# Performance work log

Hardware: AMD Instinct MI355X
Metric: run time of the kernel (lower is better)

The kernel has to match this reference:

```python
import jax, jax.numpy as jnp
import numpy as np

EPS = 1e-5
TOP_N = 8
NUM_POINTS = 100
OUT_LO, OUT_HI = 0.0, 1.0


def setup_inputs() -> dict:
    key = jax.random.key(0)
    ks = jax.random.split(key, 7)
    B, D, M, R, MO = 2048, 8, 7, 32768, 9
    x = jax.random.normal(ks[0], (B, D), dtype=jnp.float32)
    # antecedent MF index per (rule, input); -1 means input unused in that rule
    antecedents = jax.random.randint(ks[1], (R, D), 0, M + 1) - 1  # values in [-1, M)
    consequents = jax.random.randint(ks[2], (R,), 0, MO)
    in_centers = jax.random.normal(ks[3], (D, M), dtype=jnp.float32)
    in_widths = 0.2 + 0.3 * jax.random.uniform(ks[4], (D, M), dtype=jnp.float32)
    out_centers = jax.random.uniform(ks[5], (MO,), dtype=jnp.float32)
    out_widths = 0.05 + 0.2 * jax.random.uniform(ks[6], (MO,), dtype=jnp.float32)
    return {"x": x, "antecedents": antecedents, "consequents": consequents,
            "in_centers": in_centers, "in_widths": in_widths,
            "out_centers": out_centers, "out_widths": out_widths}


def reference(x, antecedents, consequents, in_centers, in_widths, out_centers, out_widths):
    B, D = x.shape
    R = antecedents.shape[0]
    M = in_centers.shape[1]

    # Fuzzification: Gaussian input MFs, clamped like the torch module. mu: [B, D, M]
    z = (x[:, :, None] - in_centers[None, :, :]) / in_widths[None, :, :]
    mu = jnp.clip(jnp.exp(-0.5 * z * z), EPS, 1.0)

    # Rule firing strengths: product over inputs of selected memberships ([B, R]).
    # Small fixed loop over D (8) keeps peak memory at one [B, R] temp per step.
    firing = jnp.ones((B, R), dtype=x.dtype)
    for i in range(D):
        idx = antecedents[:, i]                      # [R], -1 => unused
        safe = jnp.clip(idx, 0, M - 1)
        vals = mu[:, i, safe]                        # [B, R]
        firing = firing * jnp.where(idx[None, :] == -1, jnp.ones((), x.dtype), vals)

    top_vals, top_idx = jax.lax.top_k(firing, TOP_N)  # [B, TOP_N]

    # Output universe and output MF table: [MO, P]
    universe = jnp.linspace(OUT_LO, OUT_HI, NUM_POINTS, dtype=x.dtype)
    zo = (universe[None, :] - out_centers[:, None]) / out_widths[:, None]
    out_mu = jnp.exp(-0.5 * zo * zo)

    # Mamdani implication (product) + aggregation (sum) + centroid defuzzification
    cons_top = consequents[top_idx]                   # [B, TOP_N]
    implications = top_vals[:, :, None] * out_mu[cons_top]  # [B, TOP_N, P]
    aggregated = implications.sum(axis=1)             # [B, P]
    numerator = (universe[None, :] * aggregated).sum(axis=1)
    denominator = aggregated.sum(axis=1) + EPS
    return numerator / denominator
```

## Files before the change

kernel.cpp:

```cpp
#include <hip/hip_runtime.h>
#include <math.h>

#define DD 8
#define MM 7
#define MOO 9
#define NPTS 100
#define EPSF 1e-5f

#define THREADS 1024
#define ITERS 8
#define ROWS 8
#define CAP 256
#define THR_SLACK 0.9879f

__device__ __forceinline__ float bl(unsigned u) { return __uint_as_float(u << 16); }
__device__ __forceinline__ float bh(unsigned u) { return __uint_as_float(u & 0xFFFF0000u); }
__device__ __forceinline__ unsigned pkb(float a, float b) {
    return (__float_as_uint(b) & 0xFFFF0000u) | (__float_as_uint(a) >> 16);
}

__global__ __launch_bounds__(256) void pack_kernel(const int* __restrict__ ant,
                                                   unsigned* __restrict__ g_off,
                                                   int R) {
    int r = blockIdx.x * 256 + threadIdx.x;
    if (r < R) {
        const int4* a = reinterpret_cast<const int4*>(ant) + (size_t)r * 2;
        int4 lo = a[0], hi = a[1];
        int v[8] = {lo.x, lo.y, lo.z, lo.w, hi.x, hi.y, hi.z, hi.w};
        unsigned code = 0u;
        #pragma unroll
        for (int i = 0; i < 8; ++i) {
            int c = v[i];
            c = (c < 0) ? 7 : (c > MM - 1 ? MM - 1 : c);
            code |= (unsigned)c << (3 * i);
        }
        g_off[r] = ((code & 4095u) << 3) | ((((code >> 12) << 3) + 32768u) << 16);
    }
}

__global__ __launch_bounds__(THREADS, 4) void anfis_fused8(
    const float* __restrict__ x,
    const unsigned* __restrict__ stream_off,
    const int* __restrict__ consequents,
    const float* __restrict__ in_centers,
    const float* __restrict__ in_widths,
    const float* __restrict__ out_centers,
    const float* __restrict__ out_widths,
    float* __restrict__ out)
{
    __shared__ uint4 quads[8192];
    __shared__ float mu[ROWS][64];
    __shared__ float pairs[ROWS][256];
    __shared__ uint4 smaxpk[THREADS];
    __shared__ float s0s[MOO], s1s[MOO];
    __shared__ float sT[ROWS];
    __shared__ int   scnt[ROWS];
    __shared__ int   wlcnt;
    __shared__ float wv[ROWS][8];
    __shared__ int   wc[ROWS][8];

    const int tid = threadIdx.x;
    const int b0  = blockIdx.x * ROWS;

    unsigned short* wl = (unsigned short*)quads;
    float* cvals = (float*)(quads + 1024);
    int*   cidx  = (int*)(quads + 1536);

    if (tid < 512) {
        int row = tid >> 6, d = (tid >> 3) & 7, c = tid & 7;
        float v = 1.0f;
        if (c < MM) {
            float z = (x[(b0 + row) * DD + d] - in_centers[d * MM + c]) / in_widths[d * MM + c];
            v = expf(-0.5f * z * z);
            v = fminf(v, 1.0f);
            v = fmaxf(v, EPSF);
        }
        mu[row][(d << 3) + c] = v;
    } else if (tid < 512 + MOO) {
        int mo = tid - 512;
        float oc = out_centers[mo], ow = out_widths[mo];
        float s0 = 0.0f, s1 = 0.0f;
        for (int p = 0; p < NPTS; ++p) {
            float u = (float)p * (1.0f / 99.0f);
            float z = (u - oc) / ow;
            float e = expf(-0.5f * z * z);
            s0 += e;
            s1 += u * e;
        }
        s0s[mo] = s0;
        s1s[mo] = s1;
    } else if (tid >= 544 && tid < 544 + ROWS) {
        scnt[tid - 544] = 0;
    } else if (tid == 560) {
        wlcnt = 0;
    }
    __syncthreads();

    #pragma unroll
    for (int i = 0; i < 2; ++i) {
        int k = tid + i * THREADS;
        int row = k >> 8, e = k & 255;
        int p = e >> 6, q = e & 63;
        pairs[row][e] = mu[row][(2 * p) * 8 + (q & 7)] * mu[row][(2 * p + 1) * 8 + (q >> 3)];
    }
    __syncthreads();

    #pragma unroll
    for (int i = 0; i < 8; ++i) {
        int k = tid + i * THREADS;
        int t = k & 4095, h = k >> 12;
        int ia = h * 128 + (t & 63), ib = h * 128 + 64 + ((t >> 6) & 63);
        float q0 = pairs[0][ia] * pairs[0][ib];
        float q1 = pairs[1][ia] * pairs[1][ib];
        float q2 = pairs[2][ia] * pairs[2][ib];
        float q3 = pairs[3][ia] * pairs[3][ib];
        float q4 = pairs[4][ia] * pairs[4][ib];
        float q5 = pairs[5][ia] * pairs[5][ib];
        float q6 = pairs[6][ia] * pairs[6][ib];
        float q7 = pairs[7][ia] * pairs[7][ib];
        quads[k] = make_uint4(pkb(q0, q1), pkb(q2, q3), pkb(q4, q5), pkb(q6, q7));
    }
    __syncthreads();

    const uint4* pk4 = reinterpret_cast<const uint4*>(stream_off);
    float m[ROWS];
    #pragma unroll
    for (int r = 0; r < ROWS; ++r) m[r] = -1.0f;
    #pragma unroll
    for (int j = 0; j < ITERS; ++j) {
        uint4 cd = pk4[j * THREADS + tid];
        unsigned wrd[4] = {cd.x, cd.y, cd.z, cd.w};
        #pragma unroll
        for (int s = 0; s < 4; ++s) {
            unsigned w = wrd[s];
            uint4 eA = quads[(w & 0xFFFFu) >> 3];
            uint4 eB = quads[w >> 19];
            m[0] = fmaxf(m[0], bl(eA.x) * bl(eB.x));
            m[1] = fmaxf(m[1], bh(eA.x) * bh(eB.x));
            m[2] = fmaxf(m[2], bl(eA.y) * bl(eB.y));
            m[3] = fmaxf(m[3], bh(eA.y) * bh(eB.y));
            m[4] = fmaxf(m[4], bl(eA.z) * bl(eB.z));
            m[5] = fmaxf(m[5], bh(eA.z) * bh(eB.z));
            m[6] = fmaxf(m[6], bl(eA.w) * bl(eB.w));
            m[7] = fmaxf(m[7], bh(eA.w) * bh(eB.w));
        }
    }
    smaxpk[tid] = make_uint4(pkb(m[0], m[1]), pkb(m[2], m[3]),
                             pkb(m[4], m[5]), pkb(m[6], m[7]));
    __syncthreads();

    if (tid < 512) {
        int row = tid >> 6, lane = tid & 63;
        float mm[16];
        #pragma unroll
        for (int k = 0; k < 16; ++k) {
            uint4 e = smaxpk[lane + 64 * k];
            unsigned word = (row & 4) ? ((row & 2) ? e.w : e.z)
                                      : ((row & 2) ? e.y : e.x);
            mm[k] = (row & 1) ? bh(word) : bl(word);
        }
        float thr = -1.0f;
        #pragma unroll
        for (int round = 0; round < 8; ++round) {
            float lm = mm[0];
            #pragma unroll
            for (int k = 1; k < 16; ++k) lm = fmaxf(lm, mm[k]);
            float wm = lm;
            #pragma unroll
            for (int off = 32; off >= 1; off >>= 1)
                wm = fmaxf(wm, __shfl_xor(wm, off, 64));
            unsigned long long bal = __ballot(lm == wm);
            int first = (int)__ffsll(bal) - 1;
            if (lane == first) {
                bool done = false;
                #pragma unroll
                for (int k = 0; k < 16; ++k) {
                    bool rm = (!done) && (mm[k] == wm);
                    mm[k] = rm ? -2.0f : mm[k];
                    done = done || rm;
                }
            }
            thr = wm;
        }
        if (lane == 0) sT[row] = thr;
    }
    __syncthreads();

    {
        #pragma unroll
        for (int row = 0; row < ROWS; ++row) {
            if (m[row] >= THR_SLACK * sT[row]) {
                int pos = atomicAdd(&wlcnt, 1);
                wl[pos] = (unsigned short)((row << 10) | tid);
            }
        }
    }
    __syncthreads();

    {
        const int hl = tid & 31;
        const int j = hl >> 2, s = hl & 3;
        const int n = wlcnt;
        for (int i = (tid >> 5); i < n; i += 32) {
            int it  = wl[i];
            int row = it >> 10;
            int t   = it & 1023;
            int flat = (j * THREADS + t) * 4 + s;
            unsigned w = stream_off[flat];
            unsigned lo12 = (w & 0xFFFFu) >> 3;
            unsigned hi12 = (w >> 19) - 4096u;
            const float* P = pairs[row];
            float f = (P[lo12 & 63u] * P[64 + (lo12 >> 6)])
                    * (P[128 + (hi12 & 63u)] * P[192 + (hi12 >> 6)]);
            if (f >= sT[row]) {
                int pos = atomicAdd(&scnt[row], 1);
                if (pos < CAP) {
                    cvals[row * CAP + pos] = f;
                    cidx[row * CAP + pos]  = flat;
                }
            }
        }
    }
    __syncthreads();

    if (tid < 512) {
        int row = tid >> 6, lane = tid & 63;
        int n = scnt[row] < CAP ? scnt[row] : CAP;
        for (int c = lane; c < n; c += 64) {
            float v  = cvals[row * CAP + c];
            int   id = cidx[row * CAP + c];
            int rk = 0;
            for (int mI = 0; mI < n; ++mI) {
                float vm = cvals[row * CAP + mI];
                int   im = cidx[row * CAP + mI];
                rk += ((vm > v) || (vm == v && im < id)) ? 1 : 0;
            }
            if (rk < 8) {
                wv[row][rk] = v;
                wc[row][rk] = consequents[id];
            }
        }
    }
    __syncthreads();

    if (tid < ROWS) {
        int row = tid;
        float num = 0.0f, den = 0.0f;
        #pragma unroll
        for (int k = 0; k < 8; ++k) {
            num += wv[row][k] * s1s[wc[row][k]];
            den += wv[row][k] * s0s[wc[row][k]];
        }
        out[b0 + row] = num / (den + EPSF);
    }
}

__global__ __launch_bounds__(256) void anfis_kernel(
    const float* __restrict__ x,
    const int* __restrict__ ant,
    const int* __restrict__ consequents,
    const float* __restrict__ in_centers,
    const float* __restrict__ in_widths,
    const float* __restrict__ out_centers,
    const float* __restrict__ out_widths,
    float* __restrict__ out,
    int R)
{
    __shared__ float mu[64];
    __shared__ float pairs[256];
    __shared__ float s0s[MOO], s1s[MOO];
    __shared__ float svals[256][9];
    __shared__ int   sidx[256][9];

    const int tid = threadIdx.x;
    const int b   = blockIdx.x;

    if (tid < 64) {
        int d = tid >> 3, c = tid & 7;
        float v = 1.0f;
        if (c < MM) {
            float z = (x[b * DD + d] - in_centers[d * MM + c]) / in_widths[d * MM + c];
            v = expf(-0.5f * z * z);
            v = fminf(v, 1.0f);
            v = fmaxf(v, EPSF);
        }
        mu[tid] = v;
    } else if (tid < 64 + MOO) {
        int mo = tid - 64;
        float oc = out_centers[mo], ow = out_widths[mo];
        float s0 = 0.0f, s1 = 0.0f;
        for (int p = 0; p < NPTS; ++p) {
            float u = (float)p * (1.0f / 99.0f);
            float z = (u - oc) / ow;
            float e = expf(-0.5f * z * z);
            s0 += e;
            s1 += u * e;
        }
        s0s[mo] = s0;
        s1s[mo] = s1;
    }
    __syncthreads();

    {
        int p = tid >> 6, q = tid & 63;
        pairs[tid] = mu[(2 * p) * 8 + (q & 7)] * mu[(2 * p + 1) * 8 + (q >> 3)];
    }
    __syncthreads();

    float vals[8];
    int   idxs[8];
    #pragma unroll
    for (int k = 0; k < 8; ++k) { vals[k] = -1.0f; idxs[k] = 0x7fffffff; }

    for (int r = tid; r < R; r += 256) {
        const int4* a = reinterpret_cast<const int4*>(ant) + (size_t)r * 2;
        int4 lo = a[0], hi = a[1];
        int v[8] = {lo.x, lo.y, lo.z, lo.w, hi.x, hi.y, hi.z, hi.w};
        unsigned code = 0u;
        #pragma unroll
        for (int i = 0; i < 8; ++i) {
            int c = v[i];
            c = (c < 0) ? 7 : (c > MM - 1 ? MM - 1 : c);
            code |= (unsigned)c << (3 * i);
        }
        float f = pairs[code & 63]
                * pairs[64  + ((code >> 6)  & 63)]
                * pairs[128 + ((code >> 12) & 63)]
                * pairs[192 + ((code >> 18) & 63)];
        if (f > vals[7]) {
            float nv = f; int ni = r;
            #pragma unroll
            for (int k = 0; k < 8; ++k) {
                bool take = nv > vals[k];
                float cv = vals[k]; int ci = idxs[k];
                vals[k] = take ? nv : cv;
                idxs[k] = take ? ni : ci;
                nv = take ? cv : nv;
                ni = take ? ci : ni;
            }
        }
    }

    #pragma unroll
    for (int k = 0; k < 8; ++k) { svals[tid][k] = vals[k]; sidx[tid][k] = idxs[k]; }

    for (int off = 128; off >= 1; off >>= 1) {
        __syncthreads();
        if (tid < off) {
            float ov[8]; int oi[8];
            int pa = 0, pb = 0;
            #pragma unroll
            for (int k = 0; k < 8; ++k) {
                float va = svals[tid][pa];        int ia = sidx[tid][pa];
                float vb = svals[tid + off][pb];  int ib = sidx[tid + off][pb];
                bool ta = (va > vb) || ((va == vb) && (ia < ib));
                ov[k] = ta ? va : vb;
                oi[k] = ta ? ia : ib;
                pa += ta ? 1 : 0;
                pb += ta ? 0 : 1;
            }
            #pragma unroll
            for (int k = 0; k < 8; ++k) { svals[tid][k] = ov[k]; sidx[tid][k] = oi[k]; }
        }
    }
    __syncthreads();

    if (tid == 0) {
        float num = 0.0f, den = 0.0f;
        #pragma unroll
        for (int k = 0; k < 8; ++k) {
            float v = svals[0][k];
            int   c = consequents[sidx[0][k]];
            num += v * s1s[c];
            den += v * s0s[c];
        }
        out[b] = num / (den + EPSF);
    }
}

extern "C" void kernel_launch(void* const* d_in, const int* in_sizes, int n_in,
                              void* d_out, int out_size, void* d_ws, size_t ws_size,
                              hipStream_t stream) {
    const float* x      = (const float*)d_in[0];
    const int*   ant    = (const int*)d_in[1];
    const int*   cons   = (const int*)d_in[2];
    const float* in_c   = (const float*)d_in[3];
    const float* in_w   = (const float*)d_in[4];
    const float* out_c  = (const float*)d_in[5];
    const float* out_w  = (const float*)d_in[6];
    float*       out    = (float*)d_out;

    const int B = in_sizes[0] / DD;
    const int R = in_sizes[1] / DD;

    const bool shape_ok = (R == THREADS * 4 * ITERS) && (B % ROWS == 0);
    const size_t need = (size_t)R * 4;

    if (shape_ok && d_ws && ws_size >= need) {
        unsigned* g_off = (unsigned*)d_ws;
        pack_kernel<<<(R + 255) / 256, 256, 0, stream>>>(ant, g_off, R);
        anfis_fused8<<<B / ROWS, THREADS, 0, stream>>>(x, g_off, cons, in_c, in_w,
                                                       out_c, out_w, out);
    } else {
        anfis_kernel<<<B, 256, 0, stream>>>(x, ant, cons, in_c, in_w,
                                            out_c, out_w, out, R);
    }
}
```

Baseline: 36.16 us.

## Batch LDS quad reads with inline asm and move output MF sums off critical path

The main rule-scan loop now issues sixteen ds_read_b128 loads through inline asm using raw LDS byte addresses, then waits once on lgkmcnt before doing the multiply-max work, so more loads are in flight at a time. The packed offset encoding drops its premultiply-by-8 shift, and both the scan and the verify pass are updated to match. The quad table build reuses the A-side pair values across four iterations to cut LDS reads. The output-MF sum loop moves from the first phase to the threshold phase, so it no longer lengthens the critical path at the first barrier. The asm path uses more registers, which could lower occupancy.

```diff
diff --git a/kernel.cpp b/kernel.cpp
--- a/kernel.cpp
+++ b/kernel.cpp
@@ -12,6 +12,8 @@
 #define ROWS 8
 #define CAP 256
 #define THR_SLACK 0.9879f
+
+typedef unsigned uint32x4 __attribute__((ext_vector_type(4)));
 
 __device__ __forceinline__ float bl(unsigned u) { return __uint_as_float(u << 16); }
 __device__ __forceinline__ float bh(unsigned u) { return __uint_as_float(u & 0xFFFF0000u); }
@@ -34,7 +36,7 @@
             c = (c < 0) ? 7 : (c > MM - 1 ? MM - 1 : c);
             code |= (unsigned)c << (3 * i);
         }
-        g_off[r] = ((code & 4095u) << 3) | ((((code >> 12) << 3) + 32768u) << 16);
+        g_off[r] = (code & 4095u) | (((code >> 12) + 4096u) << 16);
     }
 }
 
@@ -76,19 +78,6 @@
             v = fmaxf(v, EPSF);
         }
         mu[row][(d << 3) + c] = v;
-    } else if (tid < 512 + MOO) {
-        int mo = tid - 512;
-        float oc = out_centers[mo], ow = out_widths[mo];
-        float s0 = 0.0f, s1 = 0.0f;
-        for (int p = 0; p < NPTS; ++p) {
-            float u = (float)p * (1.0f / 99.0f);
-            float z = (u - oc) / ow;
-            float e = expf(-0.5f * z * z);
-            s0 += e;
-            s1 += u * e;
-        }
-        s0s[mo] = s0;
-        s1s[mo] = s1;
     } else if (tid >= 544 && tid < 544 + ROWS) {
         scnt[tid - 544] = 0;
     } else if (tid == 560) {
@@ -106,43 +95,60 @@
     __syncthreads();
 
     #pragma unroll
-    for (int i = 0; i < 8; ++i) {
-        int k = tid + i * THREADS;
-        int t = k & 4095, h = k >> 12;
-        int ia = h * 128 + (t & 63), ib = h * 128 + 64 + ((t >> 6) & 63);
-        float q0 = pairs[0][ia] * pairs[0][ib];
-        float q1 = pairs[1][ia] * pairs[1][ib];
-        float q2 = pairs[2][ia] * pairs[2][ib];
-        float q3 = pairs[3][ia] * pairs[3][ib];
-        float q4 = pairs[4][ia] * pairs[4][ib];
-        float q5 = pairs[5][ia] * pairs[5][ib];
-        float q6 = pairs[6][ia] * pairs[6][ib];
-        float q7 = pairs[7][ia] * pairs[7][ib];
-        quads[k] = make_uint4(pkb(q0, q1), pkb(q2, q3), pkb(q4, q5), pkb(q6, q7));
+    for (int h = 0; h < 2; ++h) {
+        float a8[ROWS];
+        const int ia = h * 128 + (tid & 63);
+        #pragma unroll
+        for (int r = 0; r < ROWS; ++r) a8[r] = pairs[r][ia];
+        #pragma unroll
+        for (int ii = 0; ii < 4; ++ii) {
+            int k = tid + (h * 4 + ii) * THREADS;
+            int ib = h * 128 + 64 + ((((tid >> 6) + 16 * ii)) & 63);
+            float q0 = a8[0] * pairs[0][ib];
+            float q1 = a8[1] * pairs[1][ib];
+            float q2 = a8[2] * pairs[2][ib];
+            float q3 = a8[3] * pairs[3][ib];
+            float q4 = a8[4] * pairs[4][ib];
+            float q5 = a8[5] * pairs[5][ib];
+            float q6 = a8[6] * pairs[6][ib];
+            float q7 = a8[7] * pairs[7][ib];
+            quads[k] = make_uint4(pkb(q0, q1), pkb(q2, q3), pkb(q4, q5), pkb(q6, q7));
+        }
     }
     __syncthreads();
 
     const uint4* pk4 = reinterpret_cast<const uint4*>(stream_off);
+    const unsigned qbase = (unsigned)(uintptr_t)&quads[0];
     float m[ROWS];
     #pragma unroll
     for (int r = 0; r < ROWS; ++r) m[r] = -1.0f;
     #pragma unroll
-    for (int j = 0; j < ITERS; ++j) {
-        uint4 cd = pk4[j * THREADS + tid];
-        unsigned wrd[4] = {cd.x, cd.y, cd.z, cd.w};
-        #pragma unroll
-        for (int s = 0; s < 4; ++s) {
-            unsigned w = wrd[s];
-            uint4 eA = quads[(w & 0xFFFFu) >> 3];
-            uint4 eB = quads[w >> 19];
-            m[0] = fmaxf(m[0], bl(eA.x) * bl(eB.x));
-            m[1] = fmaxf(m[1], bh(eA.x) * bh(eB.x));
-            m[2] = fmaxf(m[2], bl(eA.y) * bl(eB.y));
-            m[3] = fmaxf(m[3], bh(eA.y) * bh(eB.y));
-            m[4] = fmaxf(m[4], bl(eA.z) * bl(eB.z));
-            m[5] = fmaxf(m[5], bh(eA.z) * bh(eB.z));
-            m[6] = fmaxf(m[6], bl(eA.w) * bl(eB.w));
-            m[7] = fmaxf(m[7], bh(eA.w) * bh(eB.w));
+    for (int half = 0; half < 4; ++half) {
+        uint4 cA = pk4[(2 * half) * THREADS + tid];
+        uint4 cB = pk4[(2 * half + 1) * THREADS + tid];
+        unsigned w[8] = {cA.x, cA.y, cA.z, cA.w, cB.x, cB.y, cB.z, cB.w};
+        uint32x4 eA[8], eB[8];
+        #pragma unroll
+        for (int s = 0; s < 8; ++s) {
+            unsigned alo = qbase + ((w[s] & 0xFFFFu) << 4);
+            unsigned ahi = qbase + ((w[s] >> 16) << 4);
+            asm volatile("ds_read_b128 %0, %1" : "=v"(eA[s]) : "v"(alo));
+            asm volatile("ds_read_b128 %0, %1" : "=v"(eB[s]) : "v"(ahi));
+        }
+        __builtin_amdgcn_sched_barrier(0);
+        asm volatile("s_waitcnt lgkmcnt(0)" ::: "memory");
+        __builtin_amdgcn_sched_barrier(0);
+        #pragma unroll
+        for (int s = 0; s < 8; ++s) {
+            uint32x4 a = eA[s], b = eB[s];
+            m[0] = fmaxf(m[0], bl(a[0]) * bl(b[0]));
+            m[1] = fmaxf(m[1], bh(a[0]) * bh(b[0]));
+            m[2] = fmaxf(m[2], bl(a[1]) * bl(b[1]));
+            m[3] = fmaxf(m[3], bh(a[1]) * bh(b[1]));
+            m[4] = fmaxf(m[4], bl(a[2]) * bl(b[2]));
+            m[5] = fmaxf(m[5], bh(a[2]) * bh(b[2]));
+            m[6] = fmaxf(m[6], bl(a[3]) * bl(b[3]));
+            m[7] = fmaxf(m[7], bh(a[3]) * bh(b[3]));
         }
     }
     smaxpk[tid] = make_uint4(pkb(m[0], m[1]), pkb(m[2], m[3]),
@@ -183,6 +189,19 @@
             thr = wm;
         }
         if (lane == 0) sT[row] = thr;
+    } else if (tid < 512 + MOO) {
+        int mo = tid - 512;
+        float oc = out_centers[mo], ow = out_widths[mo];
+        float s0 = 0.0f, s1 = 0.0f;
+        for (int p = 0; p < NPTS; ++p) {
+            float u = (float)p * (1.0f / 99.0f);
+            float z = (u - oc) / ow;
+            float e = expf(-0.5f * z * z);
+            s0 += e;
+            s1 += u * e;
+        }
+        s0s[mo] = s0;
+        s1s[mo] = s1;
     }
     __syncthreads();
 
@@ -207,8 +226,8 @@
             int t   = it & 1023;
             int flat = (j * THREADS + t) * 4 + s;
             unsigned w = stream_off[flat];
-            unsigned lo12 = (w & 0xFFFFu) >> 3;
-            unsigned hi12 = (w >> 19) - 4096u;
+            unsigned lo12 = w & 0xFFFFu;
+            unsigned hi12 = (w >> 16) - 4096u;
             const float* P = pairs[row];
             float f = (P[lo12 & 63u] * P[64 + (lo12 >> 6)])
                     * (P[128 + (hi12 & 63u)] * P[192 + (hi12 >> 6)]);
```

New measurement: 32.84 us (median of 2 runs). 9.2% less time.
